# Performance work log

Measured on AMD Instinct MI355X. Metric: run time of the kernel, lower is better.

## Reference

```python
import jax, jax.numpy as jnp
import numpy as np

B, N, NPOINT, NSAMPLE, D_IN = 8, 8192, 2048, 32, 32
RADIUS = 0.4
EPS = 1e-5


def fps(xyz, npoint):
    # xyz: [B,N,3] -> idx [B,npoint] (furthest point sampling, start at index 0)
    b, n, _ = xyz.shape
    d0 = jnp.full((b, n), 1e10, xyz.dtype)
    f0 = jnp.zeros((b,), jnp.int32)

    def step(carry, _):
        dist, far = carry
        centroid = jnp.take_along_axis(xyz, far[:, None, None].astype(jnp.int32), axis=1)  # [B,1,3]
        d = jnp.sum((xyz - centroid) ** 2, axis=-1)  # [B,N]
        dist = jnp.minimum(dist, d)
        nxt = jnp.argmax(dist, axis=-1).astype(jnp.int32)
        return (dist, nxt), far

    _, idx = jax.lax.scan(step, (d0, f0), None, length=npoint)
    return idx.T  # [B,npoint]


def ball_query(xyz, new_xyz, radius, nsample):
    # xyz [B,N,3], new_xyz [B,S,3] -> idx [B,S,nsample]
    n = xyz.shape[1]
    d2 = jnp.sum((new_xyz[:, :, None, :] - xyz[:, None, :, :]) ** 2, axis=-1)  # [B,S,N]
    cand = jnp.where(d2 <= radius * radius, jnp.arange(n, dtype=jnp.int32)[None, None, :], n)
    idx = jnp.sort(cand, axis=-1)[..., :nsample]  # first nsample in-ball indices
    first = idx[..., :1]
    idx = jnp.where(idx == n, first, idx)  # pad with first hit (CUDA ball_query semantics)
    return jnp.clip(idx, 0, n - 1)


def mlp_layer(x, w, b, g, beta):
    # x [B,S,K,Cin]; conv1x1 + training-mode BatchNorm2d + ReLU
    y = jnp.einsum('bskc,oc->bsko', x, w) + b
    mu = jnp.mean(y, axis=(0, 1, 2))
    var = jnp.var(y, axis=(0, 1, 2))
    y = (y - mu) * jax.lax.rsqrt(var + EPS) * g + beta
    return jax.nn.relu(y)


def setup_inputs() -> dict:
    key = jax.random.key(0)
    ks = jax.random.split(key, 8)
    c0 = D_IN + 3  # use_xyz concat
    return {
        'xyz': jax.random.normal(ks[0], (B, 3, N), jnp.float32),
        'points': jax.random.normal(ks[1], (B, D_IN, N), jnp.float32),
        'w1': jax.random.normal(ks[2], (64, c0), jnp.float32) * (1.0 / np.sqrt(c0)),
        'b1': jax.random.normal(ks[3], (64,), jnp.float32) * 0.01,
        'g1': jnp.ones((64,), jnp.float32),
        'be1': jnp.zeros((64,), jnp.float32),
        'w2': jax.random.normal(ks[4], (128, 64), jnp.float32) * (1.0 / np.sqrt(64)),
        'b2': jax.random.normal(ks[5], (128,), jnp.float32) * 0.01,
        'g2': jnp.ones((128,), jnp.float32),
        'be2': jnp.zeros((128,), jnp.float32),
    }


def reference(xyz, points, w1, b1, g1, be1, w2, b2, g2, be2):
    xyz_t = jnp.transpose(xyz, (0, 2, 1))  # [B,N,3]
    fps_idx = fps(xyz_t, NPOINT)  # [B,S]
    new_xyz_t = jnp.take_along_axis(xyz_t, fps_idx[..., None], axis=1)  # [B,S,3]
    idx = ball_query(xyz_t, new_xyz_t, RADIUS, NSAMPLE)  # [B,S,K]

    bidx = jnp.arange(B)[:, None, None]
    grouped_xyz = xyz_t[bidx, idx] - new_xyz_t[:, :, None, :]  # [B,S,K,3] relative coords
    feat_t = jnp.transpose(points, (0, 2, 1))  # [B,N,D]
    grouped_feat = feat_t[bidx, idx]  # [B,S,K,D]
    x = jnp.concatenate([grouped_xyz, grouped_feat], axis=-1)  # [B,S,K,3+D]

    x = mlp_layer(x, w1, b1, g1, be1)
    x = mlp_layer(x, w2, b2, g2, be2)
    new_points_res = jnp.max(x, axis=2)  # max over nsample -> [B,S,C_out]

    new_xyz = jnp.transpose(new_xyz_t, (0, 2, 1))  # [B,3,S]
    return new_xyz, jnp.transpose(new_points_res, (0, 2, 1))  # [B,C_out,S]
```

## Files before the change

kernel.cpp:

```cpp
#include <hip/hip_runtime.h>
#include <cstddef>

constexpr int B_ = 8;
constexpr int N_ = 8192;
constexpr int NPOINT_ = 2048;
constexpr int NSAMPLE_ = 32;
constexpr int DIN_ = 32;
constexpr int C1_ = 64;
constexpr int C2_ = 128;
constexpr float EPS_ = 1e-5f;
constexpr int TOT_ = B_ * NPOINT_ * NSAMPLE_;

#define FT 512
__global__ __attribute__((amdgpu_waves_per_eu(2, 2)))
__launch_bounds__(FT) void k_fps_tr(const float* __restrict__ xyz,
                                    const float* __restrict__ pts,
                                    float* __restrict__ featT,
                                    float* __restrict__ nxT,
                                    float* __restrict__ out0) {
  const int tid = threadIdx.x;

  __shared__ float4 cP[N_];
  __shared__ unsigned long long slot[2];
  __shared__ float tile[DIN_][64 + 1];

  if (blockIdx.x >= 8) {
    for (int bn = (int)blockIdx.x - 8; bn < B_ * (N_ / 64); bn += (int)gridDim.x - 8) {
      const int b = bn >> 7;
      const int n0 = (bn & 127) * 64;
      __syncthreads();
#pragma unroll
      for (int i = 0; i < 4; i++) {
        const int id = i * 512 + tid;
        const int c = id >> 6, nn = id & 63;
        tile[c][nn] = pts[((size_t)b * DIN_ + c) * N_ + n0 + nn];
      }
      __syncthreads();
#pragma unroll
      for (int i = 0; i < 4; i++) {
        const int id = i * 512 + tid;
        const int nn = id >> 5, c = id & 31;
        featT[((size_t)(b * N_ + n0 + nn)) * DIN_ + c] = tile[c][nn];
      }
    }
    return;
  }

  const int b = blockIdx.x;
  const int lane = tid & 63;
  const float* xb = xyz + (size_t)b * 3 * N_;

#define DECL(j)                                   \
  float pX##j = xb[tid + j * FT];                 \
  float pY##j = xb[N_ + tid + j * FT];            \
  float pZ##j = xb[2 * N_ + tid + j * FT];        \
  float pD##j = 1e10f;
  DECL(0) DECL(1) DECL(2) DECL(3) DECL(4) DECL(5) DECL(6) DECL(7)
  DECL(8) DECL(9) DECL(10) DECL(11) DECL(12) DECL(13) DECL(14) DECL(15)
#undef DECL

#define FILL(j) cP[tid + j * FT] = make_float4(pX##j, pY##j, pZ##j, 0.f);
  FILL(0) FILL(1) FILL(2) FILL(3) FILL(4) FILL(5) FILL(6) FILL(7)
  FILL(8) FILL(9) FILL(10) FILL(11) FILL(12) FILL(13) FILL(14) FILL(15)
#undef FILL

  asm volatile("" : "+v"(pX0), "+v"(pY0), "+v"(pZ0), "+v"(pX1), "+v"(pY1), "+v"(pZ1),
                    "+v"(pX2), "+v"(pY2), "+v"(pZ2), "+v"(pX3), "+v"(pY3), "+v"(pZ3));
  asm volatile("" : "+v"(pX4), "+v"(pY4), "+v"(pZ4), "+v"(pX5), "+v"(pY5), "+v"(pZ5),
                    "+v"(pX6), "+v"(pY6), "+v"(pZ6), "+v"(pX7), "+v"(pY7), "+v"(pZ7));
  asm volatile("" : "+v"(pX8), "+v"(pY8), "+v"(pZ8), "+v"(pX9), "+v"(pY9), "+v"(pZ9),
                    "+v"(pX10), "+v"(pY10), "+v"(pZ10), "+v"(pX11), "+v"(pY11), "+v"(pZ11));
  asm volatile("" : "+v"(pX12), "+v"(pY12), "+v"(pZ12), "+v"(pX13), "+v"(pY13), "+v"(pZ13),
                    "+v"(pX14), "+v"(pY14), "+v"(pZ14), "+v"(pX15), "+v"(pY15), "+v"(pZ15));

  if (tid == 0) { slot[0] = 0ull; slot[1] = 0ull; }
  __syncthreads();

#define UPDASM(j)                                                   \
  "v_sub_f32 %[t0], %[px" #j "], %[cx]\n\t"                         \
  "v_sub_f32 %[t1], %[py" #j "], %[cy]\n\t"                         \
  "v_sub_f32 %[t2], %[pz" #j "], %[cz]\n\t"                         \
  "v_mul_f32 %[t0], %[t0], %[t0]\n\t"                               \
  "v_mul_f32 %[t1], %[t1], %[t1]\n\t"                               \
  "v_mul_f32 %[t2], %[t2], %[t2]\n\t"                               \
  "v_add_f32 %[t0], %[t0], %[t1]\n\t"                               \
  "v_add_f32 %[t0], %[t0], %[t2]\n\t"                               \
  "v_min_f32 %[pd" #j "], %[pd" #j "], %[t0]\n\t"                   \
  "v_cmp_le_f32 vcc, %[pd" #j "], %[lv]\n\t"                        \
  "v_max_f32 %[lv], %[lv], %[pd" #j "]\n\t"                         \
  "v_cndmask_b32 %[js], " #j ", %[js], vcc\n\t"

#define DPPR(op, v, ctrl)                                                        \
  #op " %[" #v "], %[" #v "], %[" #v "] " ctrl                                   \
  " row_mask:0xf bank_mask:0xf bound_ctrl:0\n\t"                                 \
  "s_nop 1\n\t"

  int far = 0;
  int h0 = 0, h1 = 0, h2 = 0, h3 = 0;
  for (int s = 0; s < NPOINT_ - 1; ++s) {
    const float4 c = cP[far];
    const float cx = c.x, cy = c.y, cz = c.z;

    float lv = 0.0f;
    int js = 0;
    float t0, t1, t2;
    asm volatile(
        UPDASM(0) UPDASM(1) UPDASM(2) UPDASM(3)
        UPDASM(4) UPDASM(5) UPDASM(6) UPDASM(7)
        UPDASM(8) UPDASM(9) UPDASM(10) UPDASM(11)
        UPDASM(12) UPDASM(13) UPDASM(14) UPDASM(15)
        : [pd0] "+v"(pD0), [pd1] "+v"(pD1), [pd2] "+v"(pD2), [pd3] "+v"(pD3),
          [pd4] "+v"(pD4), [pd5] "+v"(pD5), [pd6] "+v"(pD6), [pd7] "+v"(pD7),
          [pd8] "+v"(pD8), [pd9] "+v"(pD9), [pd10] "+v"(pD10), [pd11] "+v"(pD11),
          [pd12] "+v"(pD12), [pd13] "+v"(pD13), [pd14] "+v"(pD14), [pd15] "+v"(pD15),
          [lv] "+v"(lv), [js] "+v"(js),
          [t0] "=&v"(t0), [t1] "=&v"(t1), [t2] "=&v"(t2)
        : [px0] "v"(pX0), [py0] "v"(pY0), [pz0] "v"(pZ0),
          [px1] "v"(pX1), [py1] "v"(pY1), [pz1] "v"(pZ1),
          [px2] "v"(pX2), [py2] "v"(pY2), [pz2] "v"(pZ2),
          [px3] "v"(pX3), [py3] "v"(pY3), [pz3] "v"(pZ3),
          [px4] "v"(pX4), [py4] "v"(pY4), [pz4] "v"(pZ4),
          [px5] "v"(pX5), [py5] "v"(pY5), [pz5] "v"(pZ5),
          [px6] "v"(pX6), [py6] "v"(pY6), [pz6] "v"(pZ6),
          [px7] "v"(pX7), [py7] "v"(pY7), [pz7] "v"(pZ7),
          [px8] "v"(pX8), [py8] "v"(pY8), [pz8] "v"(pZ8),
          [px9] "v"(pX9), [py9] "v"(pY9), [pz9] "v"(pZ9),
          [px10] "v"(pX10), [py10] "v"(pY10), [pz10] "v"(pZ10),
          [px11] "v"(pX11), [py11] "v"(pY11), [pz11] "v"(pZ11),
          [px12] "v"(pX12), [py12] "v"(pY12), [pz12] "v"(pZ12),
          [px13] "v"(pX13), [py13] "v"(pY13), [pz13] "v"(pZ13),
          [px14] "v"(pX14), [py14] "v"(pY14), [pz14] "v"(pZ14),
          [px15] "v"(pX15), [py15] "v"(pY15), [pz15] "v"(pZ15),
          [cx] "v"(cx), [cy] "v"(cy), [cz] "v"(cz)
        : "vcc");
    const int li13 = 8191 - (tid + (js << 9));

    int smi;
    int key = 0;
    float red;
    asm volatile(
        "v_mov_b32 %[red], %[lv]\n\t"
        "s_nop 1\n\t"
        DPPR(v_max_f32, red, "row_ror:1")
        DPPR(v_max_f32, red, "row_ror:2")
        DPPR(v_max_f32, red, "row_ror:4")
        DPPR(v_max_f32, red, "row_ror:8")
        DPPR(v_max_f32, red, "row_bcast:15")
        DPPR(v_max_f32, red, "row_bcast:31")
        "s_nop 3\n\t"
        "v_readlane_b32 %[sm], %[red], 63\n\t"
        "s_nop 3\n\t"
        "v_cmp_eq_f32 vcc, %[sm], %[lv]\n\t"
        "v_cndmask_b32 %[key], 0, %[li13], vcc\n\t"
        "s_nop 1\n\t"
        DPPR(v_max_u32, key, "row_ror:1")
        DPPR(v_max_u32, key, "row_ror:2")
        DPPR(v_max_u32, key, "row_ror:4")
        DPPR(v_max_u32, key, "row_ror:8")
        DPPR(v_max_u32, key, "row_bcast:15")
        DPPR(v_max_u32, key, "row_bcast:31")
        : [red] "=&v"(red), [sm] "=&s"(smi), [key] "+v"(key)
        : [lv] "v"(lv), [li13] "v"(li13)
        : "vcc");

    if (lane == 63) {
      const unsigned long long pk = ((unsigned long long)s << 45) |
                                    ((unsigned long long)(unsigned)smi << 13) |
                                    (unsigned)key;
      atomicMax(&slot[s & 1], pk);
    }
    __syncthreads();
    far = 8191 - (int)(slot[s & 1] & 0x1FFFull);

    const int d = s + 1 - tid;
    if (d == 0) h0 = far;
    if (d == 512) h1 = far;
    if (d == 1024) h2 = far;
    if (d == 1536) h3 = far;
  }
#undef UPDASM
#undef DPPR

  {
#define WOUT(k, hh)                                                   \
    {                                                                 \
      const int ss = tid + (k) * FT;                                  \
      const float4 cc = cP[hh];                                       \
      nxT[(size_t)(b * NPOINT_ + ss) * 3 + 0] = cc.x;                 \
      nxT[(size_t)(b * NPOINT_ + ss) * 3 + 1] = cc.y;                 \
      nxT[(size_t)(b * NPOINT_ + ss) * 3 + 2] = cc.z;                 \
      out0[((size_t)b * 3 + 0) * NPOINT_ + ss] = cc.x;                \
      out0[((size_t)b * 3 + 1) * NPOINT_ + ss] = cc.y;                \
      out0[((size_t)b * 3 + 2) * NPOINT_ + ss] = cc.z;                \
    }
    WOUT(0, h0) WOUT(1, h1) WOUT(2, h2) WOUT(3, h3)
#undef WOUT
  }
}

__global__ __launch_bounds__(256) void k_ballquery(const float* __restrict__ xyz,
                                                   const float* __restrict__ nxT,
                                                   int* __restrict__ gidx) {
  const int wid = (int)((blockIdx.x * 256 + threadIdx.x) >> 6);
  const int lane = threadIdx.x & 63;
  const int b = wid >> 11;
  const float* xb = xyz + (size_t)b * 3 * N_;
  const float cx = nxT[(size_t)wid * 3 + 0];
  const float cy = nxT[(size_t)wid * 3 + 1];
  const float cz = nxT[(size_t)wid * 3 + 2];
  int* out = gidx + (size_t)wid * NSAMPLE_;

  int count = 0, first = 0;
  for (int ch = 0; ch < N_ / 64; ++ch) {
    const int j = ch * 64 + lane;
    const float dx = xb[j] - cx, dy = xb[N_ + j] - cy, dz = xb[2 * N_ + j] - cz;
    const float d2 = __fadd_rn(__fadd_rn(__fmul_rn(dx, dx), __fmul_rn(dy, dy)),
                               __fmul_rn(dz, dz));
    const bool in = (d2 <= 0.16f);
    const unsigned long long mask = __ballot(in);
    if (mask) {
      if (count == 0) first = ch * 64 + (__ffsll((long long)mask) - 1);
      if (in) {
        const int rank = count + __popcll(mask & ((1ull << lane) - 1ull));
        if (rank < NSAMPLE_) out[rank] = j;
      }
      count += __popcll(mask);
      if (count >= NSAMPLE_) break;
    }
  }
  if (count < NSAMPLE_ && lane >= count && lane < NSAMPLE_) out[lane] = first;
}

#define XS(k, c) xs[(k) * 36 + (c)]

template <int PHASE>
__global__ __launch_bounds__(256) void k_mlp(
    const float* __restrict__ xyz, const float* __restrict__ featT,
    const float* __restrict__ nxT, const int* __restrict__ gidx,
    const float* __restrict__ w1, const float* __restrict__ b1,
    const float* __restrict__ w2, const float* __restrict__ b2,
    const float* __restrict__ ac1,
    float* __restrict__ part, float* __restrict__ maxb, float* __restrict__ minb) {
  extern __shared__ float smem[];
  float* xs = smem;
  float* w1s = smem + 1152;
  float* w2cm = smem + 1152 + 2240;
  float* x2s = w2cm + 8192;
  float* pbuf = (PHASE == 1) ? (smem + 1152 + 2240) : (x2s + 2048);

  const int t = threadIdx.x;
  for (int i = t; i < 64 * 35; i += 256) w1s[i] = w1[i];
  if constexpr (PHASE == 2) {
    for (int i = t; i < 64 * 128; i += 256) {
      const int c = i >> 7, o = i & 127;
      w2cm[i] = w2[o * 64 + c];
    }
  }
  const int o2 = t & 31, kq = t >> 5;
  const int gk = t >> 3, gq = t & 7;

  float bb1[2];
  float a1r[2] = {0.f, 0.f}, c1r[2] = {0.f, 0.f};
  float bb2[4] = {0.f, 0.f, 0.f, 0.f};
#pragma unroll
  for (int q = 0; q < 2; q++) bb1[q] = b1[o2 * 2 + q];
  if constexpr (PHASE == 2) {
#pragma unroll
    for (int q = 0; q < 2; q++) { a1r[q] = ac1[o2 * 2 + q]; c1r[q] = ac1[64 + o2 * 2 + q]; }
#pragma unroll
    for (int q = 0; q < 4; q++) bb2[q] = b2[o2 * 4 + q];
  }

  float s1a[2] = {0.f, 0.f}, s1q[2] = {0.f, 0.f};
  float s2a[4] = {0.f, 0.f, 0.f, 0.f}, s2q[4] = {0.f, 0.f, 0.f, 0.f};

  float4 fpre;
  float xpx = 0.f, xpy = 0.f, xpz = 0.f;
  {
    const int G = blockIdx.x * 8;
    const int b = G >> 11;
    const int j = gidx[(size_t)G * NSAMPLE_ + gk];
    fpre = *(const float4*)(featT + ((size_t)(b * N_ + j)) * DIN_ + gq * 4);
    if (t < 32) {
      const int j2 = gidx[(size_t)G * NSAMPLE_ + t];
      const float* xb = xyz + (size_t)b * 3 * N_;
      xpx = xb[j2] - nxT[(size_t)G * 3 + 0];
      xpy = xb[N_ + j2] - nxT[(size_t)G * 3 + 1];
      xpz = xb[2 * N_ + j2] - nxT[(size_t)G * 3 + 2];
    }
  }

  for (int i = 0; i < 8; i++) {
    const int G = blockIdx.x * 8 + i;
    __syncthreads();
    XS(gk, 3 + gq * 4 + 0) = fpre.x;
    XS(gk, 3 + gq * 4 + 1) = fpre.y;
    XS(gk, 3 + gq * 4 + 2) = fpre.z;
    XS(gk, 3 + gq * 4 + 3) = fpre.w;
    if (t < 32) { XS(t, 0) = xpx; XS(t, 1) = xpy; XS(t, 2) = xpz; }
    if (i < 7) {
      const int Gn = G + 1;
      const int bn = Gn >> 11;
      const int jn = gidx[(size_t)Gn * NSAMPLE_ + gk];
      fpre = *(const float4*)(featT + ((size_t)(bn * N_ + jn)) * DIN_ + gq * 4);
      if (t < 32) {
        const int j2 = gidx[(size_t)Gn * NSAMPLE_ + t];
        const float* xb = xyz + (size_t)bn * 3 * N_;
        xpx = xb[j2] - nxT[(size_t)Gn * 3 + 0];
        xpy = xb[N_ + j2] - nxT[(size_t)Gn * 3 + 1];
        xpz = xb[2 * N_ + j2] - nxT[(size_t)Gn * 3 + 2];
      }
    }
    __syncthreads();

    float acc[4][2];
#pragma unroll
    for (int r = 0; r < 4; r++) { acc[r][0] = bb1[0]; acc[r][1] = bb1[1]; }
#pragma unroll
    for (int c = 0; c < 35; c++) {
      float xv[4];
#pragma unroll
      for (int r = 0; r < 4; r++) xv[r] = XS(kq * 4 + r, c);
      float wv[2];
      wv[0] = w1s[(o2 * 2 + 0) * 35 + c];
      wv[1] = w1s[(o2 * 2 + 1) * 35 + c];
#pragma unroll
      for (int r = 0; r < 4; r++) { acc[r][0] += xv[r] * wv[0]; acc[r][1] += xv[r] * wv[1]; }
    }

    if constexpr (PHASE == 1) {
#pragma unroll
      for (int q = 0; q < 2; q++)
#pragma unroll
        for (int r = 0; r < 4; r++) {
          const float v = acc[r][q];
          s1a[q] += v;
          s1q[q] += v * v;
        }
    } else {
#pragma unroll
      for (int r = 0; r < 4; r++)
#pragma unroll
        for (int q = 0; q < 2; q++) {
          float v = acc[r][q] * a1r[q] + c1r[q];
          v = fmaxf(v, 0.f);
          x2s[(kq * 4 + r) * 64 + o2 * 2 + q] = v;
        }
      __syncthreads();

      float a2[4][4];
#pragma unroll
      for (int r = 0; r < 4; r++)
#pragma unroll
        for (int q = 0; q < 4; q++) a2[r][q] = bb2[q];
#pragma unroll 4
      for (int cc4 = 0; cc4 < 16; cc4++) {
        float4 xv4[4];
#pragma unroll
        for (int r = 0; r < 4; r++) xv4[r] = *(const float4*)&x2s[(kq * 4 + r) * 64 + cc4 * 4];
        float4 wv4[4];
#pragma unroll
        for (int cq = 0; cq < 4; cq++) wv4[cq] = *(const float4*)&w2cm[(cc4 * 4 + cq) * 128 + o2 * 4];
#pragma unroll
        for (int cq = 0; cq < 4; cq++) {
#pragma unroll
          for (int r = 0; r < 4; r++) {
            const float xr = ((const float*)&xv4[r])[cq];
#pragma unroll
            for (int q = 0; q < 4; q++) a2[r][q] += xr * ((const float*)&wv4[cq])[q];
          }
        }
      }

#pragma unroll
      for (int q = 0; q < 4; q++)
#pragma unroll
        for (int r = 0; r < 4; r++) {
          const float v = a2[r][q];
          s2a[q] += v;
          s2q[q] += v * v;
        }
      float mx[4], mn[4];
#pragma unroll
      for (int q = 0; q < 4; q++) { mx[q] = a2[0][q]; mn[q] = a2[0][q]; }
#pragma unroll
      for (int r = 1; r < 4; r++)
#pragma unroll
        for (int q = 0; q < 4; q++) {
          mx[q] = fmaxf(mx[q], a2[r][q]);
          mn[q] = fminf(mn[q], a2[r][q]);
        }
#pragma unroll
      for (int q = 0; q < 4; q++) {
        pbuf[kq * 128 + o2 * 4 + q] = mx[q];
        pbuf[1024 + kq * 128 + o2 * 4 + q] = mn[q];
      }
      __syncthreads();
      if (t < 128) {
        float MX = pbuf[t], MN = pbuf[1024 + t];
#pragma unroll
        for (int kk = 1; kk < 8; kk++) {
          MX = fmaxf(MX, pbuf[kk * 128 + t]);
          MN = fminf(MN, pbuf[1024 + kk * 128 + t]);
        }
        maxb[(size_t)G * 128 + t] = MX;
        minb[(size_t)G * 128 + t] = MN;
      }
    }
  }

  if constexpr (PHASE == 1) {
    __syncthreads();
#pragma unroll
    for (int q = 0; q < 2; q++) {
      pbuf[(o2 * 2 + q) * 8 + kq] = s1a[q];
      pbuf[512 + (o2 * 2 + q) * 8 + kq] = s1q[q];
    }
    __syncthreads();
    if (t < 64) {
      float S = 0.f, Q = 0.f;
#pragma unroll
      for (int kk = 0; kk < 8; kk++) { S += pbuf[t * 8 + kk]; Q += pbuf[512 + t * 8 + kk]; }
      part[(size_t)blockIdx.x * 128 + t * 2 + 0] = S;
      part[(size_t)blockIdx.x * 128 + t * 2 + 1] = Q;
    }
  }
  if constexpr (PHASE == 2) {
    __syncthreads();
#pragma unroll
    for (int q = 0; q < 4; q++) {
      pbuf[(o2 * 4 + q) * 8 + kq] = s2a[q];
      pbuf[1024 + (o2 * 4 + q) * 8 + kq] = s2q[q];
    }
    __syncthreads();
    if (t < 128) {
      float S = 0.f, Q = 0.f;
#pragma unroll
      for (int kk = 0; kk < 8; kk++) { S += pbuf[t * 8 + kk]; Q += pbuf[1024 + t * 8 + kk]; }
      part[(size_t)blockIdx.x * 256 + t * 2 + 0] = S;
      part[(size_t)blockIdx.x * 256 + t * 2 + 1] = Q;
    }
  }
}

__global__ __launch_bounds__(1024) void k_stats1(const float* __restrict__ part,
                                                 const float* __restrict__ g,
                                                 const float* __restrict__ be,
                                                 float* __restrict__ ac) {
  const int t = threadIdx.x;
  const int ch = t & 63, sl = t >> 6;
  float s = 0.f, q = 0.f;
  for (int bk = sl; bk < 2048; bk += 16) {
    const float2 v = *(const float2*)(part + (size_t)bk * 128 + ch * 2);
    s += v.x;
    q += v.y;
  }
  __shared__ float ss[16][64], qs[16][64];
  ss[sl][ch] = s;
  qs[sl][ch] = q;
  __syncthreads();
  if (t < 64) {
    float S = 0.f, Q = 0.f;
#pragma unroll
    for (int k = 0; k < 16; k++) { S += ss[k][t]; Q += qs[k][t]; }
    const float mu = S / (float)TOT_;
    const float var = Q / (float)TOT_ - mu * mu;
    const float a = g[t] * (1.0f / sqrtf(var + EPS_));
    ac[t] = a;
    ac[64 + t] = be[t] - mu * a;
  }
}

__global__ __launch_bounds__(1024) void k_stats2(const float* __restrict__ part,
                                                 const float* __restrict__ g,
                                                 const float* __restrict__ be,
                                                 float* __restrict__ ac) {
  const int t = threadIdx.x;
  const int ch = t & 127, sl = t >> 7;
  float s = 0.f, q = 0.f;
  for (int bk = sl; bk < 2048; bk += 8) {
    const float2 v = *(const float2*)(part + (size_t)bk * 256 + ch * 2);
    s += v.x;
    q += v.y;
  }
  __shared__ float ss[8][128], qs[8][128];
  ss[sl][ch] = s;
  qs[sl][ch] = q;
  __syncthreads();
  if (t < 128) {
    float S = 0.f, Q = 0.f;
#pragma unroll
    for (int k = 0; k < 8; k++) { S += ss[k][t]; Q += qs[k][t]; }
    const float mu = S / (float)TOT_;
    const float var = Q / (float)TOT_ - mu * mu;
    const float a = g[t] * (1.0f / sqrtf(var + EPS_));
    ac[t] = a;
    ac[128 + t] = be[t] - mu * a;
  }
}

__global__ __launch_bounds__(256) void k_finalize(const float* __restrict__ maxb,
                                                  const float* __restrict__ minb,
                                                  const float* __restrict__ ac2,
                                                  float* __restrict__ out1) {
  __shared__ float tile[128][33];
  const int b = blockIdx.x >> 6;
  const int s0 = (blockIdx.x & 63) * 32;
  const int t = threadIdx.x;
#pragma unroll
  for (int it = 0; it < 16; ++it) {
    const int idx = it * 256 + t;
    const int sl = idx >> 7, ch = idx & 127;
    const size_t G = (size_t)b * NPOINT_ + s0 + sl;
    const float a = ac2[ch], c = ac2[128 + ch];
    const float y = (a >= 0.f) ? maxb[G * 128 + ch] : minb[G * 128 + ch];
    tile[ch][sl] = fmaxf(y * a + c, 0.f);
  }
  __syncthreads();
#pragma unroll
  for (int it = 0; it < 16; ++it) {
    const int idx = it * 256 + t;
    const int ch = idx >> 5, sl = idx & 31;
    out1[((size_t)(b * C2_ + ch)) * NPOINT_ + s0 + sl] = tile[ch][sl];
  }
}

extern "C" void kernel_launch(void* const* d_in, const int* in_sizes, int n_in,
                              void* d_out, int out_size, void* d_ws, size_t ws_size,
                              hipStream_t stream) {
  const float* xyz = (const float*)d_in[0];
  const float* pts = (const float*)d_in[1];
  const float* w1 = (const float*)d_in[2];
  const float* b1 = (const float*)d_in[3];
  const float* g1 = (const float*)d_in[4];
  const float* be1 = (const float*)d_in[5];
  const float* w2 = (const float*)d_in[6];
  const float* b2 = (const float*)d_in[7];
  const float* g2 = (const float*)d_in[8];
  const float* be2 = (const float*)d_in[9];

  float* out0 = (float*)d_out;
  float* out1 = out0 + (size_t)B_ * 3 * NPOINT_;

  float* wsf = (float*)d_ws;
  float* featT = wsf;
  float* nxT = featT + (size_t)B_ * N_ * DIN_;
  float* part1 = nxT + (size_t)B_ * NPOINT_ * 3;
  float* part2 = part1 + (size_t)2048 * 128;
  float* ac1 = part2 + (size_t)2048 * 256;
  float* ac2 = ac1 + 128;
  float* maxb = ac2 + 256;
  float* minb = maxb + (size_t)B_ * NPOINT_ * 128;
  int* gidx = (int*)(minb + (size_t)B_ * NPOINT_ * 128);

  const size_t smem1 = (size_t)(1152 + 2240 + 2048) * 4;
  const size_t smem2 = (size_t)(1152 + 2240 + 8192 + 2048 + 2048) * 4;

  k_fps_tr<<<dim3(256), dim3(FT), 0, stream>>>(xyz, pts, featT, nxT, out0);
  k_ballquery<<<dim3(B_ * NPOINT_ / 4), dim3(256), 0, stream>>>(xyz, nxT, gidx);
  k_mlp<1><<<dim3(2048), dim3(256), smem1, stream>>>(xyz, featT, nxT, gidx, w1, b1, w2, b2,
                                                     nullptr, part1, nullptr, nullptr);
  k_stats1<<<dim3(1), dim3(1024), 0, stream>>>(part1, g1, be1, ac1);
  k_mlp<2><<<dim3(2048), dim3(256), smem2, stream>>>(xyz, featT, nxT, gidx, w1, b1, w2, b2,
                                                     ac1, part2, maxb, minb);
  k_stats2<<<dim3(1), dim3(1024), 0, stream>>>(part2, g2, be2, ac2);
  k_finalize<<<dim3(B_ * (NPOINT_ / 32)), dim3(256), 0, stream>>>(maxb, minb, ac2, out1);
}
```

Before: 2.078 ms.

## Overlap ball query and layer-1 stats with FPS in a persistent megakernel

The separate ball-query and phase-1 MLP kernels are folded into the idle 248 blocks of the FPS kernel. FPS blocks publish 256-centroid chunks through global flags, and worker waves spin on those flags so they can run the ball query and the layer-1 conv statistics while FPS is still going. Each wave keeps one output channel's weights in registers and writes per-wave partial sums, and stats1 now reduces over waves instead of blocks. This removes two launches and their serial time, but it depends on all 256 blocks being co-resident and adds spin-wait traffic and atomics.

```diff
diff --git a/kernel.cpp b/kernel.cpp
--- a/kernel.cpp
+++ b/kernel.cpp
@@ -10,14 +10,24 @@
 constexpr int C2_ = 128;
 constexpr float EPS_ = 1e-5f;
 constexpr int TOT_ = B_ * NPOINT_ * NSAMPLE_;
+constexpr int NWAVE_ = 248 * 8;
+
+__global__ void k_init(unsigned* __restrict__ sync) {
+  if (threadIdx.x < 65) sync[threadIdx.x] = 0u;
+}
 
 #define FT 512
 __global__ __attribute__((amdgpu_waves_per_eu(2, 2)))
-__launch_bounds__(FT) void k_fps_tr(const float* __restrict__ xyz,
-                                    const float* __restrict__ pts,
-                                    float* __restrict__ featT,
-                                    float* __restrict__ nxT,
-                                    float* __restrict__ out0) {
+__launch_bounds__(FT) void k_mega(const float* __restrict__ xyz,
+                                  const float* __restrict__ pts,
+                                  float* __restrict__ featT,
+                                  float* __restrict__ nxT,
+                                  float* __restrict__ out0,
+                                  int* __restrict__ gidx,
+                                  const float* __restrict__ w1,
+                                  const float* __restrict__ b1,
+                                  float* __restrict__ part1,
+                                  unsigned* __restrict__ sync) {
   const int tid = threadIdx.x;
 
   __shared__ float4 cP[N_];
@@ -43,6 +53,88 @@
         featT[((size_t)(b * N_ + n0 + nn)) * DIN_ + c] = tile[c][nn];
       }
     }
+    __syncthreads();
+    if (tid == 0) __hip_atomic_fetch_add(&sync[64], 1u, __ATOMIC_RELEASE, __HIP_MEMORY_SCOPE_AGENT);
+    while (__hip_atomic_load(&sync[64], __ATOMIC_ACQUIRE, __HIP_MEMORY_SCOPE_AGENT) < 248u)
+      __builtin_amdgcn_s_sleep(16);
+
+    const int wv = tid >> 6;
+    const int lane = tid & 63;
+    float* xs = (float*)cP + wv * 1152;
+    int* jiw = (int*)((float*)cP + 8 * 1152) + wv * 32;
+
+    float wreg[35];
+#pragma unroll
+    for (int c = 0; c < 35; c++) wreg[c] = w1[lane * 35 + c];
+    const float bb = b1[lane];
+
+    float s1a = 0.f, s1q = 0.f;
+    const int W = ((int)blockIdx.x - 8) * 8 + wv;
+
+    for (int G = W; G < B_ * NPOINT_; G += NWAVE_) {
+      while (__hip_atomic_load(&sync[G >> 8], __ATOMIC_ACQUIRE, __HIP_MEMORY_SCOPE_AGENT) == 0u)
+        __builtin_amdgcn_s_sleep(16);
+
+      const int b = G >> 11;
+      const float* xb = xyz + (size_t)b * 3 * N_;
+      const float cx = nxT[(size_t)G * 3 + 0];
+      const float cy = nxT[(size_t)G * 3 + 1];
+      const float cz = nxT[(size_t)G * 3 + 2];
+      int* out = gidx + (size_t)G * NSAMPLE_;
+
+      int count = 0, first = 0;
+      for (int ch = 0; ch < N_ / 64; ++ch) {
+        const int j = ch * 64 + lane;
+        const float dx = xb[j] - cx, dy = xb[N_ + j] - cy, dz = xb[2 * N_ + j] - cz;
+        const float d2 = __fadd_rn(__fadd_rn(__fmul_rn(dx, dx), __fmul_rn(dy, dy)),
+                                   __fmul_rn(dz, dz));
+        const bool in = (d2 <= 0.16f);
+        const unsigned long long mask = __ballot(in);
+        if (mask) {
+          if (count == 0) first = ch * 64 + (__ffsll((long long)mask) - 1);
+          if (in) {
+            const int rank = count + __popcll(mask & ((1ull << lane) - 1ull));
+            if (rank < NSAMPLE_) { out[rank] = j; jiw[rank] = j; }
+          }
+          count += __popcll(mask);
+          if (count >= NSAMPLE_) break;
+        }
+      }
+      if (count < NSAMPLE_ && lane >= count && lane < NSAMPLE_) {
+        out[lane] = first;
+        jiw[lane] = first;
+      }
+
+      {
+        const int k = lane & 31, half = lane >> 5;
+        const int j = jiw[k];
+        if (half == 0) {
+          xs[k * 36 + 0] = xb[j] - cx;
+          xs[k * 36 + 1] = xb[N_ + j] - cy;
+          xs[k * 36 + 2] = xb[2 * N_ + j] - cz;
+        }
+#pragma unroll
+        for (int q = 0; q < 4; q++) {
+          const int slotq = half * 4 + q;
+          const float4 v =
+              *(const float4*)(featT + ((size_t)(b * N_ + j)) * DIN_ + slotq * 4);
+          xs[k * 36 + 3 + slotq * 4 + 0] = v.x;
+          xs[k * 36 + 3 + slotq * 4 + 1] = v.y;
+          xs[k * 36 + 3 + slotq * 4 + 2] = v.z;
+          xs[k * 36 + 3 + slotq * 4 + 3] = v.w;
+        }
+      }
+
+      for (int k = 0; k < 32; k++) {
+        float y = bb;
+#pragma unroll
+        for (int c = 0; c < 35; c++) y = fmaf(xs[k * 36 + c], wreg[c], y);
+        s1a += y;
+        s1q += y * y;
+      }
+    }
+    part1[(size_t)W * 128 + lane * 2 + 0] = s1a;
+    part1[(size_t)W * 128 + lane * 2 + 1] = s1q;
     return;
   }
 
@@ -177,6 +269,23 @@
     if (d == 512) h1 = far;
     if (d == 1024) h2 = far;
     if (d == 1536) h3 = far;
+
+    if ((s & 255) == 254) {
+      const int w = s >> 8;
+      const int kk = w >> 1;
+      const int tlo = (w & 1) * 256;
+      if (tid >= tlo && tid < tlo + 256) {
+        const int hh = (kk == 0) ? h0 : (kk == 1) ? h1 : (kk == 2) ? h2 : h3;
+        const float4 cc = cP[hh];
+        const int ss = tid + kk * 512;
+        float* dst = nxT + (size_t)(b * NPOINT_ + ss) * 3;
+        dst[0] = cc.x; dst[1] = cc.y; dst[2] = cc.z;
+      }
+      __syncthreads();
+      if (tid == 0)
+        __hip_atomic_store(&sync[b * 8 + w], 1u, __ATOMIC_RELEASE,
+                           __HIP_MEMORY_SCOPE_AGENT);
+    }
   }
 #undef UPDASM
 #undef DPPR
@@ -196,45 +305,14 @@
     WOUT(0, h0) WOUT(1, h1) WOUT(2, h2) WOUT(3, h3)
 #undef WOUT
   }
+  __syncthreads();
+  if (tid == 0)
+    __hip_atomic_store(&sync[b * 8 + 7], 1u, __ATOMIC_RELEASE,
+                       __HIP_MEMORY_SCOPE_AGENT);
 }
 
-__global__ __launch_bounds__(256) void k_ballquery(const float* __restrict__ xyz,
-                                                   const float* __restrict__ nxT,
-                                                   int* __restrict__ gidx) {
-  const int wid = (int)((blockIdx.x * 256 + threadIdx.x) >> 6);
-  const int lane = threadIdx.x & 63;
-  const int b = wid >> 11;
-  const float* xb = xyz + (size_t)b * 3 * N_;
-  const float cx = nxT[(size_t)wid * 3 + 0];
-  const float cy = nxT[(size_t)wid * 3 + 1];
-  const float cz = nxT[(size_t)wid * 3 + 2];
-  int* out = gidx + (size_t)wid * NSAMPLE_;
-
-  int count = 0, first = 0;
-  for (int ch = 0; ch < N_ / 64; ++ch) {
-    const int j = ch * 64 + lane;
-    const float dx = xb[j] - cx, dy = xb[N_ + j] - cy, dz = xb[2 * N_ + j] - cz;
-    const float d2 = __fadd_rn(__fadd_rn(__fmul_rn(dx, dx), __fmul_rn(dy, dy)),
-                               __fmul_rn(dz, dz));
-    const bool in = (d2 <= 0.16f);
-    const unsigned long long mask = __ballot(in);
-    if (mask) {
-      if (count == 0) first = ch * 64 + (__ffsll((long long)mask) - 1);
-      if (in) {
-        const int rank = count + __popcll(mask & ((1ull << lane) - 1ull));
-        if (rank < NSAMPLE_) out[rank] = j;
-      }
-      count += __popcll(mask);
-      if (count >= NSAMPLE_) break;
-    }
-  }
-  if (count < NSAMPLE_ && lane >= count && lane < NSAMPLE_) out[lane] = first;
-}
-
 #define XS(k, c) xs[(k) * 36 + (c)]
-
-template <int PHASE>
-__global__ __launch_bounds__(256) void k_mlp(
+__global__ __launch_bounds__(256) void k_mlp2(
     const float* __restrict__ xyz, const float* __restrict__ featT,
     const float* __restrict__ nxT, const int* __restrict__ gidx,
     const float* __restrict__ w1, const float* __restrict__ b1,
@@ -246,32 +324,27 @@
   float* w1s = smem + 1152;
   float* w2cm = smem + 1152 + 2240;
   float* x2s = w2cm + 8192;
-  float* pbuf = (PHASE == 1) ? (smem + 1152 + 2240) : (x2s + 2048);
+  float* pbuf = x2s + 2048;
 
   const int t = threadIdx.x;
   for (int i = t; i < 64 * 35; i += 256) w1s[i] = w1[i];
-  if constexpr (PHASE == 2) {
-    for (int i = t; i < 64 * 128; i += 256) {
-      const int c = i >> 7, o = i & 127;
-      w2cm[i] = w2[o * 64 + c];
-    }
+  for (int i = t; i < 64 * 128; i += 256) {
+    const int c = i >> 7, o = i & 127;
+    w2cm[i] = w2[o * 64 + c];
   }
   const int o2 = t & 31, kq = t >> 5;
   const int gk = t >> 3, gq = t & 7;
 
-  float bb1[2];
-  float a1r[2] = {0.f, 0.f}, c1r[2] = {0.f, 0.f};
-  float bb2[4] = {0.f, 0.f, 0.f, 0.f};
-#pragma unroll
-  for (int q = 0; q < 2; q++) bb1[q] = b1[o2 * 2 + q];
-  if constexpr (PHASE == 2) {
-#pragma unroll
-    for (int q = 0; q < 2; q++) { a1r[q] = ac1[o2 * 2 + q]; c1r[q] = ac1[64 + o2 * 2 + q]; }
-#pragma unroll
-    for (int q = 0; q < 4; q++) bb2[q] = b2[o2 * 4 + q];
-  }
-
-  float s1a[2] = {0.f, 0.f}, s1q[2] = {0.f, 0.f};
+  float bb1[2], a1r[2], c1r[2], bb2[4];
+#pragma unroll
+  for (int q = 0; q < 2; q++) {
+    bb1[q] = b1[o2 * 2 + q];
+    a1r[q] = ac1[o2 * 2 + q];
+    c1r[q] = ac1[64 + o2 * 2 + q];
+  }
+#pragma unroll
+  for (int q = 0; q < 4; q++) bb2[q] = b2[o2 * 4 + q];
+
   float s2a[4] = {0.f, 0.f, 0.f, 0.f}, s2q[4] = {0.f, 0.f, 0.f, 0.f};
 
   float4 fpre;
@@ -328,118 +401,89 @@
       for (int r = 0; r < 4; r++) { acc[r][0] += xv[r] * wv[0]; acc[r][1] += xv[r] * wv[1]; }
     }
 
-    if constexpr (PHASE == 1) {
-#pragma unroll
-      for (int q = 0; q < 2; q++)
+#pragma unroll
+    for (int r = 0; r < 4; r++)
+#pragma unroll
+      for (int q = 0; q < 2; q++) {
+        float v = acc[r][q] * a1r[q] + c1r[q];
+        v = fmaxf(v, 0.f);
+        x2s[(kq * 4 + r) * 64 + o2 * 2 + q] = v;
+      }
+    __syncthreads();
+
+    float a2[4][4];
+#pragma unroll
+    for (int r = 0; r < 4; r++)
+#pragma unroll
+      for (int q = 0; q < 4; q++) a2[r][q] = bb2[q];
+#pragma unroll 4
+    for (int cc4 = 0; cc4 < 16; cc4++) {
+      float4 xv4[4];
+#pragma unroll
+      for (int r = 0; r < 4; r++) xv4[r] = *(const float4*)&x2s[(kq * 4 + r) * 64 + cc4 * 4];
+      float4 wv4[4];
+#pragma unroll
+      for (int cq = 0; cq < 4; cq++) wv4[cq] = *(const float4*)&w2cm[(cc4 * 4 + cq) * 128 + o2 * 4];
+#pragma unroll
+      for (int cq = 0; cq < 4; cq++) {
 #pragma unroll
         for (int r = 0; r < 4; r++) {
-          const float v = acc[r][q];
-          s1a[q] += v;
-          s1q[q] += v * v;
+          const float xr = ((const float*)&xv4[r])[cq];
+#pragma unroll
+          for (int q = 0; q < 4; q++) a2[r][q] += xr * ((const float*)&wv4[cq])[q];
         }
-    } else {
-#pragma unroll
-      for (int r = 0; r < 4; r++)
-#pragma unroll
-        for (int q = 0; q < 2; q++) {
-          float v = acc[r][q] * a1r[q] + c1r[q];
-          v = fmaxf(v, 0.f);
-          x2s[(kq * 4 + r) * 64 + o2 * 2 + q] = v;
-        }
-      __syncthreads();
-
-      float a2[4][4];
-#pragma unroll
-      for (int r = 0; r < 4; r++)
-#pragma unroll
-        for (int q = 0; q < 4; q++) a2[r][q] = bb2[q];
-#pragma unroll 4
-      for (int cc4 = 0; cc4 < 16; cc4++) {
-        float4 xv4[4];
-#pragma unroll
-        for (int r = 0; r < 4; r++) xv4[r] = *(const float4*)&x2s[(kq * 4 + r) * 64 + cc4 * 4];
-        float4 wv4[4];
-#pragma unroll
-        for (int cq = 0; cq < 4; cq++) wv4[cq] = *(const float4*)&w2cm[(cc4 * 4 + cq) * 128 + o2 * 4];
-#pragma unroll
-        for (int cq = 0; cq < 4; cq++) {
-#pragma unroll
-          for (int r = 0; r < 4; r++) {
-            const float xr = ((const float*)&xv4[r])[cq];
-#pragma unroll
-            for (int q = 0; q < 4; q++) a2[r][q] += xr * ((const float*)&wv4[cq])[q];
-          }
-        }
-      }
-
-#pragma unroll
-      for (int q = 0; q < 4; q++)
-#pragma unroll
-        for (int r = 0; r < 4; r++) {
-          const float v = a2[r][q];
-          s2a[q] += v;
-          s2q[q] += v * v;
-        }
-      float mx[4], mn[4];
-#pragma unroll
-      for (int q = 0; q < 4; q++) { mx[q] = a2[0][q]; mn[q] = a2[0][q]; }
-#pragma unroll
-      for (int r = 1; r < 4; r++)
-#pragma unroll
-        for (int q = 0; q < 4; q++) {
-          mx[q] = fmaxf(mx[q], a2[r][q]);
-          mn[q] = fminf(mn[q], a2[r][q]);
-        }
+      }
+    }
+
+#pragma unroll
+    for (int q = 0; q < 4; q++)
+#pragma unroll
+      for (int r = 0; r < 4; r++) {
+        const float v = a2[r][q];
+        s2a[q] += v;
+        s2q[q] += v * v;
+      }
+    float mx[4], mn[4];
+#pragma unroll
+    for (int q = 0; q < 4; q++) { mx[q] = a2[0][q]; mn[q] = a2[0][q]; }
+#pragma unroll
+    for (int r = 1; r < 4; r++)
 #pragma unroll
       for (int q = 0; q < 4; q++) {
-        pbuf[kq * 128 + o2 * 4 + q] = mx[q];
-        pbuf[1024 + kq * 128 + o2 * 4 + q] = mn[q];
-      }
-      __syncthreads();
-      if (t < 128) {
-        float MX = pbuf[t], MN = pbuf[1024 + t];
-#pragma unroll
-        for (int kk = 1; kk < 8; kk++) {
-          MX = fmaxf(MX, pbuf[kk * 128 + t]);
-          MN = fminf(MN, pbuf[1024 + kk * 128 + t]);
-        }
-        maxb[(size_t)G * 128 + t] = MX;
-        minb[(size_t)G * 128 + t] = MN;
-      }
-    }
-  }
-
-  if constexpr (PHASE == 1) {
-    __syncthreads();
-#pragma unroll
-    for (int q = 0; q < 2; q++) {
-      pbuf[(o2 * 2 + q) * 8 + kq] = s1a[q];
-      pbuf[512 + (o2 * 2 + q) * 8 + kq] = s1q[q];
-    }
-    __syncthreads();
-    if (t < 64) {
-      float S = 0.f, Q = 0.f;
-#pragma unroll
-      for (int kk = 0; kk < 8; kk++) { S += pbuf[t * 8 + kk]; Q += pbuf[512 + t * 8 + kk]; }
-      part[(size_t)blockIdx.x * 128 + t * 2 + 0] = S;
-      part[(size_t)blockIdx.x * 128 + t * 2 + 1] = Q;
-    }
-  }
-  if constexpr (PHASE == 2) {
-    __syncthreads();
+        mx[q] = fmaxf(mx[q], a2[r][q]);
+        mn[q] = fminf(mn[q], a2[r][q]);
+      }
 #pragma unroll
     for (int q = 0; q < 4; q++) {
-      pbuf[(o2 * 4 + q) * 8 + kq] = s2a[q];
-      pbuf[1024 + (o2 * 4 + q) * 8 + kq] = s2q[q];
+      pbuf[kq * 128 + o2 * 4 + q] = mx[q];
+      pbuf[1024 + kq * 128 + o2 * 4 + q] = mn[q];
     }
     __syncthreads();
     if (t < 128) {
-      float S = 0.f, Q = 0.f;
-#pragma unroll
-      for (int kk = 0; kk < 8; kk++) { S += pbuf[t * 8 + kk]; Q += pbuf[1024 + t * 8 + kk]; }
-      part[(size_t)blockIdx.x * 256 + t * 2 + 0] = S;
-      part[(size_t)blockIdx.x * 256 + t * 2 + 1] = Q;
-    }
+      float MX = pbuf[t], MN = pbuf[1024 + t];
+#pragma unroll
+      for (int kk = 1; kk < 8; kk++) {
+        MX = fmaxf(MX, pbuf[kk * 128 + t]);
+        MN = fminf(MN, pbuf[1024 + kk * 128 + t]);
+      }
+      maxb[(size_t)G * 128 + t] = MX;
+      minb[(size_t)G * 128 + t] = MN;
+    }
+  }
+
+  __syncthreads();
+#pragma unroll
+  for (int q = 0; q < 4; q++) {
+    pbuf[(o2 * 4 + q) * 8 + kq] = s2a[q];
+    pbuf[1024 + (o2 * 4 + q) * 8 + kq] = s2q[q];
+  }
+  __syncthreads();
+  if (t < 128) {
+    float S = 0.f, Q = 0.f;
+#pragma unroll
+    for (int kk = 0; kk < 8; kk++) { S += pbuf[t * 8 + kk]; Q += pbuf[1024 + t * 8 + kk]; }
+    part[(size_t)blockIdx.x * 256 + t * 2 + 0] = S;
+    part[(size_t)blockIdx.x * 256 + t * 2 + 1] = Q;
   }
 }
 
@@ -450,7 +494,7 @@
   const int t = threadIdx.x;
   const int ch = t & 63, sl = t >> 6;
   float s = 0.f, q = 0.f;
-  for (int bk = sl; bk < 2048; bk += 16) {
+  for (int bk = sl; bk < NWAVE_; bk += 16) {
     const float2 v = *(const float2*)(part + (size_t)bk * 128 + ch * 2);
     s += v.x;
     q += v.y;
@@ -552,17 +596,16 @@
   float* maxb = ac2 + 256;
   float* minb = maxb + (size_t)B_ * NPOINT_ * 128;
   int* gidx = (int*)(minb + (size_t)B_ * NPOINT_ * 128);
-
-  const size_t smem1 = (size_t)(1152 + 2240 + 2048) * 4;
+  unsigned* sync = (unsigned*)(gidx + (size_t)B_ * NPOINT_ * NSAMPLE_);
+
   const size_t smem2 = (size_t)(1152 + 2240 + 8192 + 2048 + 2048) * 4;
 
-  k_fps_tr<<<dim3(256), dim3(FT), 0, stream>>>(xyz, pts, featT, nxT, out0);
-  k_ballquery<<<dim3(B_ * NPOINT_ / 4), dim3(256), 0, stream>>>(xyz, nxT, gidx);
-  k_mlp<1><<<dim3(2048), dim3(256), smem1, stream>>>(xyz, featT, nxT, gidx, w1, b1, w2, b2,
-                                                     nullptr, part1, nullptr, nullptr);
+  k_init<<<dim3(1), dim3(128), 0, stream>>>(sync);
+  k_mega<<<dim3(256), dim3(FT), 0, stream>>>(xyz, pts, featT, nxT, out0, gidx,
+                                             w1, b1, part1, sync);
   k_stats1<<<dim3(1), dim3(1024), 0, stream>>>(part1, g1, be1, ac1);
-  k_mlp<2><<<dim3(2048), dim3(256), smem2, stream>>>(xyz, featT, nxT, gidx, w1, b1, w2, b2,
-                                                     ac1, part2, maxb, minb);
+  k_mlp2<<<dim3(2048), dim3(256), smem2, stream>>>(xyz, featT, nxT, gidx, w1, b1, w2, b2,
+                                                   ac1, part2, maxb, minb);
   k_stats2<<<dim3(1), dim3(1024), 0, stream>>>(part2, g2, be2, ac2);
   k_finalize<<<dim3(B_ * (NPOINT_ / 32)), dim3(256), 0, stream>>>(maxb, minb, ac2, out1);
 }
```

Result: slower. 2.204 ms (+6.1%).
